# Kernel tuning notes

Measured on AMD Instinct MI355X. Metric: run time of the kernel, lower is better.

The kernel has to match this reference:

```python
import jax, jax.numpy as jnp
import numpy as np

POOL = 7; SR = 2; SCALE = 1.0 / 16
NUM_CLASSES = 21
NMS_THR = 0.5; MIN_SIZE = 1.0; TOPK = 100; SCORE_THR = 0.05
BBOX_CLIP = float(np.log(1000.0 / 16))


def roi_align(feat, rois):
    # feat: [C,H,W]; rois: [P,4] xyxy in image coords. torchvision aligned=True, sampling_ratio=2.
    C, H, W = feat.shape
    S = POOL * SR
    x0r = rois[:, 0] * SCALE - 0.5
    y0r = rois[:, 1] * SCALE - 0.5
    bw = (rois[:, 2] - rois[:, 0]) * SCALE / POOL
    bh = (rois[:, 3] - rois[:, 1]) * SCALE / POOL
    t = (jnp.arange(S, dtype=feat.dtype) + 0.5) / SR  # sample offsets in bin units
    ys = y0r[:, None] + bh[:, None] * t  # [P,S]
    xs = x0r[:, None] + bw[:, None] * t  # [P,S]
    vy = (ys >= -1.0) & (ys <= H)
    vx = (xs >= -1.0) & (xs <= W)
    y = jnp.clip(ys, 0.0, H - 1)
    x = jnp.clip(xs, 0.0, W - 1)
    yl = jnp.floor(y).astype(jnp.int32); xl = jnp.floor(x).astype(jnp.int32)
    yh = jnp.minimum(yl + 1, H - 1);     xh = jnp.minimum(xl + 1, W - 1)
    ly = y - yl; lx = x - xl
    hy = 1.0 - ly; hx = 1.0 - lx

    def g(Yi, Xi):  # -> [C,P,S,S]
        return feat[:, Yi[:, :, None], Xi[:, None, :]]

    val = (g(yl, xl) * (hy[:, :, None] * hx[:, None, :])
         + g(yl, xh) * (hy[:, :, None] * lx[:, None, :])
         + g(yh, xl) * (ly[:, :, None] * hx[:, None, :])
         + g(yh, xh) * (ly[:, :, None] * lx[:, None, :]))
    val = val * (vy[:, :, None] & vx[:, None, :])[None].astype(feat.dtype)
    P = rois.shape[0]
    val = val.reshape(C, P, POOL, SR, POOL, SR).mean(axis=(3, 5))  # avg over 2x2 samples/bin
    return val.transpose(1, 0, 2, 3)  # [P,C,POOL,POOL]


def decode(pred, proposals):
    # pred: [N,K,4] (dx,dy,dw,dh); proposals: [N,4]
    w = proposals[:, 2] - proposals[:, 0]
    h = proposals[:, 3] - proposals[:, 1]
    cx = proposals[:, 0] + 0.5 * w
    cy = proposals[:, 1] + 0.5 * h
    dx, dy = pred[..., 0], pred[..., 1]
    dw = jnp.minimum(pred[..., 2], BBOX_CLIP)
    dh = jnp.minimum(pred[..., 3], BBOX_CLIP)
    pcx = dx * w[:, None] + cx[:, None]
    pcy = dy * h[:, None] + cy[:, None]
    pw = jnp.exp(dw) * w[:, None]
    ph = jnp.exp(dh) * h[:, None]
    return jnp.stack([pcx - 0.5 * pw, pcy - 0.5 * ph, pcx + 0.5 * pw, pcy + 0.5 * ph], axis=-1)


def box_iou(b):
    x1, y1, x2, y2 = b[:, 0], b[:, 1], b[:, 2], b[:, 3]
    area = (x2 - x1) * (y2 - y1)
    iw = jnp.maximum(jnp.minimum(x2[:, None], x2[None, :]) - jnp.maximum(x1[:, None], x1[None, :]), 0.0)
    ih = jnp.maximum(jnp.minimum(y2[:, None], y2[None, :]) - jnp.maximum(y1[:, None], y1[None, :]), 0.0)
    inter = iw * ih
    return inter / (area[:, None] + area[None, :] - inter)


def filter_predictions(boxes, labels, scores):
    # score threshold + min-size + per-class greedy NMS + topK, static shapes (padded to TOPK)
    N = scores.shape[0]
    ws = boxes[:, 2] - boxes[:, 0]
    hs = boxes[:, 3] - boxes[:, 1]
    valid = (scores > SCORE_THR) & (ws >= MIN_SIZE) & (hs >= MIN_SIZE)
    skey = jnp.where(valid, scores, -jnp.inf)
    order = jnp.argsort(-skey)
    b = boxes[order]; s = skey[order]; l = labels[order]; v = valid[order]
    # batched_nms via per-class coordinate offset
    off = jax.lax.stop_gradient(jnp.max(boxes) + 1.0)
    ob = jax.lax.stop_gradient(b) + (l.astype(b.dtype) * off)[:, None]
    iou = box_iou(ob)  # [N,N]
    idx = jnp.arange(N)

    def body(keep, i):
        sup = (iou[i] > NMS_THR) & keep[i] & (idx > i)
        return keep & ~sup, None

    keep, _ = jax.lax.scan(body, v, idx)
    rank = jnp.cumsum(keep) - 1
    final = keep & (rank < TOPK)
    pick = jnp.argsort(jnp.where(final, idx, N))[:TOPK]  # kept indices in score order, padded
    ok = final[pick]
    out_boxes = jnp.where(ok[:, None], b[pick], 0.0)
    out_scores = jnp.where(ok, s[pick], 0.0)
    out_labels = jnp.where(ok, l[pick], -1)
    return out_boxes, out_labels, out_scores


def roi_head_forward(image, feat, proposals, fc6_w, fc6_b, fc7_w, fc7_b, cls_w, cls_b, reg_w, reg_b):
    H_img, W_img = image.shape[-2], image.shape[-1]
    pooled = roi_align(feat[0], proposals)  # [P,C,7,7]
    x = pooled.reshape(pooled.shape[0], -1)
    x = jax.nn.relu(x @ fc6_w.T + fc6_b)
    x = jax.nn.relu(x @ fc7_w.T + fc7_b)
    cls_scores = x @ cls_w.T + cls_b                       # [P,K]
    box_pred = (x @ reg_w.T + reg_b).reshape(-1, NUM_CLASSES, 4)
    boxes = decode(box_pred, proposals)                    # [P,K,4]
    scores = jax.nn.softmax(cls_scores, axis=-1)
    boxes = jnp.stack([boxes[..., 0].clip(0, W_img), boxes[..., 1].clip(0, H_img),
                       boxes[..., 2].clip(0, W_img), boxes[..., 3].clip(0, H_img)], axis=-1)
    labels = jnp.broadcast_to(jnp.arange(NUM_CLASSES), scores.shape)
    boxes = boxes[:, 1:].reshape(-1, 4)
    scores = scores[:, 1:].reshape(-1)
    labels = (labels[:, 1:] - 1).reshape(-1)
    return filter_predictions(boxes, labels, scores)


def setup_inputs() -> dict:
    key = jax.random.key(0)
    ks = jax.random.split(key, 12)
    H_img, W_img = 800, 1072
    P, C = 300, 512
    image = jnp.zeros((1, 3, H_img, W_img), jnp.float32)
    feat = jax.random.normal(ks[0], (1, C, H_img // 16, W_img // 16), jnp.float32)
    cx = jax.random.uniform(ks[1], (P,)) * W_img
    cy = jax.random.uniform(ks[2], (P,)) * H_img
    bw = 20.0 + jax.random.uniform(ks[3], (P,)) * 300.0
    bh = 20.0 + jax.random.uniform(ks[4], (P,)) * 300.0
    proposals = jnp.stack([jnp.clip(cx - bw / 2, 0, W_img), jnp.clip(cy - bh / 2, 0, H_img),
                           jnp.clip(cx + bw / 2, 0, W_img), jnp.clip(cy + bh / 2, 0, H_img)], axis=1)
    fin = C * POOL * POOL  # 25088
    D = 1024
    fc6_w = jax.random.normal(ks[5], (D, fin), jnp.float32) / np.sqrt(fin)
    fc6_b = jnp.zeros((D,), jnp.float32)
    fc7_w = jax.random.normal(ks[6], (D, D), jnp.float32) / np.sqrt(D)
    fc7_b = jnp.zeros((D,), jnp.float32)
    cls_w = jax.random.normal(ks[7], (NUM_CLASSES, D), jnp.float32) / np.sqrt(D)
    cls_b = jnp.zeros((NUM_CLASSES,), jnp.float32)
    reg_w = jax.random.normal(ks[8], (NUM_CLASSES * 4, D), jnp.float32) * 0.001
    reg_b = jnp.zeros((NUM_CLASSES * 4,), jnp.float32)
    return {"image": image, "feat": feat, "proposals": proposals,
            "fc6_w": fc6_w, "fc6_b": fc6_b, "fc7_w": fc7_w, "fc7_b": fc7_b,
            "cls_w": cls_w, "cls_b": cls_b, "reg_w": reg_w, "reg_b": reg_b}


def reference(image, feat, proposals, fc6_w, fc6_b, fc7_w, fc7_b, cls_w, cls_b, reg_w, reg_b):
    return roi_head_forward(image, feat, proposals, fc6_w, fc6_b, fc7_w, fc7_b, cls_w, cls_b, reg_w, reg_b)
```

## Files before the change

### kernel.cpp

```cpp
#include <hip/hip_runtime.h>
#include <hip/hip_bf16.h>
#include <math.h>

#define P_N   300
#define C_N   512
#define H_F   50
#define W_F   67
#define HW_F  3350
#define D_N   1024
#define FIN   25088
#define NCLS  21
#define NCAND 6000
#define W_IMG 1072.0f
#define H_IMG 800.0f
#define BBOX_CLIP_F 4.135166556742356f
#define KS6   42
#define STEPS6_PER_Z 19
#define KS7   16
#define STEPS7_PER_Z 2
#define KSH   16
#define STEPSH_PER_Z 2
#define NHEAD 128
#define NW    96
#define A_SCALE 16.0f
#define B_SCALE 256.0f
#define O_SCALE (1.0f / 4096.0f)

typedef __attribute__((ext_vector_type(8)))  _Float16 half8;
typedef __attribute__((ext_vector_type(16))) float    f32x16;

__device__ __forceinline__ void splitA(float f, _Float16& h, _Float16& l) {
  float fs = f * A_SCALE;
  h = (_Float16)fs;
  l = (_Float16)(fs - (float)h);
}

__global__ __launch_bounds__(256) void transpose_feat(const float* __restrict__ feat,
                                                      float* __restrict__ ft) {
  __shared__ float tile[32][33];
  const int s0 = blockIdx.x * 32, c0 = blockIdx.y * 32;
  const int tx = threadIdx.x, ty = threadIdx.y;
  for (int r = ty; r < 32; r += 8) {
    int c = c0 + r, s = s0 + tx;
    tile[r][tx] = (s < HW_F) ? feat[(size_t)c * HW_F + s] : 0.0f;
  }
  __syncthreads();
  for (int r = ty; r < 32; r += 8) {
    int s = s0 + r, c = c0 + tx;
    if (s < HW_F) ft[(size_t)s * C_N + c] = tile[tx][r];
  }
}

__global__ __launch_bounds__(256) void roi_align_k(const float* __restrict__ ft,
                                                   const float* __restrict__ rois,
                                                   _Float16* __restrict__ Xhi,
                                                   _Float16* __restrict__ Xlo) {
  __shared__ _Float16 hbuf[12544] __attribute__((aligned(16)));
  __shared__ _Float16 lbuf[12544] __attribute__((aligned(16)));
  __shared__ int   g_yl[14], g_yh[14], g_xl[14], g_xh[14];
  __shared__ float g_ly[14], g_hy[14], g_lx[14], g_hx[14];
  __shared__ int   g_vy[14], g_vx[14];

  const int p   = blockIdx.x;
  const int ch  = blockIdx.y;
  const int tid = threadIdx.x;

  if (tid < 14) {
    const float rx0 = rois[p*4+0], ry0 = rois[p*4+1], rx1 = rois[p*4+2], ry1 = rois[p*4+3];
    const float x0r = rx0 * 0.0625f - 0.5f;
    const float y0r = ry0 * 0.0625f - 0.5f;
    const float bw  = (rx1 - rx0) * 0.0625f * (1.0f / 7.0f);
    const float bh  = (ry1 - ry0) * 0.0625f * (1.0f / 7.0f);
    const float t   = ((float)tid + 0.5f) * 0.5f;

    const float ys = y0r + bh * t;
    g_vy[tid] = (ys >= -1.0f) && (ys <= (float)H_F);
    float y = fminf(fmaxf(ys, 0.0f), (float)(H_F - 1));
    int yi = (int)floorf(y);
    g_yl[tid] = yi; g_yh[tid] = min(yi + 1, H_F - 1);
    g_ly[tid] = y - (float)yi; g_hy[tid] = 1.0f - (y - (float)yi);

    const float xs = x0r + bw * t;
    g_vx[tid] = (xs >= -1.0f) && (xs <= (float)W_F);
    float x = fminf(fmaxf(xs, 0.0f), (float)(W_F - 1));
    int xi = (int)floorf(x);
    g_xl[tid] = xi; g_xh[tid] = min(xi + 1, W_F - 1);
    g_lx[tid] = x - (float)xi; g_hx[tid] = 1.0f - (x - (float)xi);
  }
  __syncthreads();

  const int c = ch * 256 + tid;
  for (int cell = 0; cell < 49; ++cell) {
    const int py = cell / 7;
    const int px = cell - py * 7;
    float acc = 0.0f;
#pragma unroll
    for (int sy = 0; sy < 2; ++sy) {
      const int iy = 2 * py + sy;
      if (!g_vy[iy]) continue;
      const float ly = g_ly[iy], hy = g_hy[iy];
      const int ry0i = g_yl[iy] * W_F, ry1i = g_yh[iy] * W_F;
#pragma unroll
      for (int sx = 0; sx < 2; ++sx) {
        const int ix = 2 * px + sx;
        if (!g_vx[ix]) continue;
        const float lx = g_lx[ix], hx = g_hx[ix];
        const float* b00 = ft + (size_t)(ry0i + g_xl[ix]) * C_N;
        const float* b01 = ft + (size_t)(ry0i + g_xh[ix]) * C_N;
        const float* b10 = ft + (size_t)(ry1i + g_xl[ix]) * C_N;
        const float* b11 = ft + (size_t)(ry1i + g_xh[ix]) * C_N;
        acc += (hy*hx)*b00[c] + (hy*lx)*b01[c] + (ly*hx)*b10[c] + (ly*lx)*b11[c];
      }
    }
    _Float16 h, l;
    splitA(acc * 0.25f, h, l);
    hbuf[tid * 49 + cell] = h;
    lbuf[tid * 49 + cell] = l;
  }
  __syncthreads();

  const size_t base = (size_t)p * FIN + (size_t)ch * 12544;
  const uint4* hs = (const uint4*)hbuf;
  const uint4* ls = (const uint4*)lbuf;
  uint4* dh = (uint4*)(Xhi + base);
  uint4* dl = (uint4*)(Xlo + base);
  for (int k = tid; k < 1568; k += 256) { dh[k] = hs[k]; dl[k] = ls[k]; }
}

__device__ __forceinline__ int swz(int slot, int ks) {
  return slot ^ ((slot >> 5) & 1) ^ (((slot >> 3) & 1) << 1) ^ ((ks & 1) << 2);
}

__global__ __launch_bounds__(256, 3) void gemm_f16_3p(
    const _Float16* __restrict__ Ahi, const _Float16* __restrict__ Alo,
    const float* __restrict__ Wt, float* __restrict__ Pt,
    int M, int K, int steps_per_z, int ldc)
{
  __shared__ _Float16 lds[16384];
  const int tid  = threadIdx.x;
  const int lane = tid & 63, wave = tid >> 6;
  const int wm = wave >> 1, wn = wave & 1;

  const int GX = gridDim.x, GY = gridDim.y;
  const int T  = GX * GY * gridDim.z;
  int flat = blockIdx.x + GX * (blockIdx.y + GY * blockIdx.z);
  if ((T & 7) == 0) flat = (flat & 7) * (T >> 3) + (flat >> 3);
  const int bx = flat % GX;
  const int by = (flat / GX) % GY;
  const int bz = flat / (GX * GY);

  const int m0 = bx * 128, n0 = by * 128;
  const int steps_total = K >> 5;
  const int s0 = bz * steps_per_z;
  const int s1 = min(s0 + steps_per_z, steps_total);

  f32x16 acc[2][2];
#pragma unroll
  for (int a = 0; a < 2; ++a)
#pragma unroll
    for (int b = 0; b < 2; ++b)
#pragma unroll
      for (int r = 0; r < 16; ++r) acc[a][b][r] = 0.f;

  const int srow = tid >> 2;
  const int j8   = tid & 3;
  const int ksW  = j8 >> 1, kc8 = j8 & 1;
  const int wslot = swz((kc8 << 5) | (srow & 31), ksW);

  for (int step = s0; step < s1; ++step) {
    const int kb = step << 5;
#pragma unroll
    for (int half = 0; half < 2; ++half) {
      const int row = srow + half * 64;
      const int mf  = row >> 5;
      const int gm  = m0 + row;
      uint4 vh = make_uint4(0,0,0,0), vl = make_uint4(0,0,0,0);
      if (gm < M) {
        vh = *reinterpret_cast<const uint4*>(Ahi + (size_t)gm * K + kb + j8 * 8);
        vl = *reinterpret_cast<const uint4*>(Alo + (size_t)gm * K + kb + j8 * 8);
      }
      const int base = (mf * 2 + ksW) * 512 + wslot * 8;
      *reinterpret_cast<uint4*>(&lds[base])        = vh;
      *reinterpret_cast<uint4*>(&lds[4096 + base]) = vl;
    }
#pragma unroll
    for (int half = 0; half < 2; ++half) {
      const int n = srow + half * 64;
      const float* wp = Wt + (size_t)(n0 + n) * K + kb + j8 * 8;
      const float4 f0 = *reinterpret_cast<const float4*>(wp);
      const float4 f1 = *reinterpret_cast<const float4*>(wp + 4);
      float fv[8] = {f0.x, f0.y, f0.z, f0.w, f1.x, f1.y, f1.z, f1.w};
      union { _Float16 h[8]; uint4 v; } uh, ul;
#pragma unroll
      for (int e = 0; e < 8; ++e) {
        float fs = fv[e] * B_SCALE;
        uh.h[e] = (_Float16)fs;
        ul.h[e] = (_Float16)(fs - (float)uh.h[e]);
      }
      const int nf = n >> 5;
      const int base = 8192 + (nf * 2 + ksW) * 512 + wslot * 8;
      *reinterpret_cast<uint4*>(&lds[base])        = uh.v;
      *reinterpret_cast<uint4*>(&lds[4096 + base]) = ul.v;
    }
    __syncthreads();
#pragma unroll
    for (int ks = 0; ks < 2; ++ks) {
      const int rslot = swz(lane, ks) * 8;
      half8 ah[2], al[2], bh[2], bl[2];
#pragma unroll
      for (int mi = 0; mi < 2; ++mi) {
        const int mf = wm * 2 + mi;
        ah[mi] = *reinterpret_cast<const half8*>(&lds[(mf * 2 + ks) * 512 + rslot]);
        al[mi] = *reinterpret_cast<const half8*>(&lds[4096 + (mf * 2 + ks) * 512 + rslot]);
      }
#pragma unroll
      for (int ni = 0; ni < 2; ++ni) {
        const int nf = wn * 2 + ni;
        bh[ni] = *reinterpret_cast<const half8*>(&lds[8192  + (nf * 2 + ks) * 512 + rslot]);
        bl[ni] = *reinterpret_cast<const half8*>(&lds[12288 + (nf * 2 + ks) * 512 + rslot]);
      }
#pragma unroll
      for (int mi = 0; mi < 2; ++mi)
#pragma unroll
        for (int ni = 0; ni < 2; ++ni) {
          acc[mi][ni] = __builtin_amdgcn_mfma_f32_32x32x16_f16(ah[mi], bh[ni], acc[mi][ni], 0, 0, 0);
          acc[mi][ni] = __builtin_amdgcn_mfma_f32_32x32x16_f16(ah[mi], bl[ni], acc[mi][ni], 0, 0, 0);
          acc[mi][ni] = __builtin_amdgcn_mfma_f32_32x32x16_f16(al[mi], bh[ni], acc[mi][ni], 0, 0, 0);
        }
    }
    __syncthreads();
  }
  const int col = lane & 31, rhi = lane >> 5;
  float* outp = Pt + (size_t)bz * ((size_t)M * ldc);
#pragma unroll
  for (int mi = 0; mi < 2; ++mi)
#pragma unroll
    for (int ni = 0; ni < 2; ++ni) {
      const int n = n0 + (wn * 2 + ni) * 32 + col;
      if (n >= ldc) continue;
#pragma unroll
      for (int r = 0; r < 16; ++r) {
        const int m = m0 + (wm * 2 + mi) * 32 + ((r & 3) + 8 * (r >> 2) + 4 * rhi);
        if (m < M) outp[(size_t)m * ldc + n] = acc[mi][ni][r] * O_SCALE;
      }
    }
}

__global__ __launch_bounds__(256) void reduce_bias(
    const float* __restrict__ Pt, const float* __restrict__ bias,
    float* __restrict__ out_f32, _Float16* __restrict__ out_hi, _Float16* __restrict__ out_lo,
    int MN, int KS, int nmask, int relu)
{
  int i = blockIdx.x * 256 + threadIdx.x;
  if (i >= MN) return;
  float s = 0.0f;
  for (int k = 0; k < KS; ++k) s += Pt[(size_t)k * MN + i];
  s += bias[i & nmask];
  if (relu) s = fmaxf(s, 0.0f);
  if (out_f32) out_f32[i] = s;
  if (out_hi) {
    _Float16 h, l; splitA(s, h, l);
    out_hi[i] = h; out_lo[i] = l;
  }
}

__global__ __launch_bounds__(256) void prep_head(const float* __restrict__ cls_w,
                                                 const float* __restrict__ cls_b,
                                                 const float* __restrict__ reg_w,
                                                 const float* __restrict__ reg_b,
                                                 float* __restrict__ Wpad,
                                                 float* __restrict__ bpad,
                                                 int* __restrict__ vcount) {
  const int row = blockIdx.x;
  const int t = threadIdx.x;
  if (row == 0 && t == 0) *vcount = 0;
  const float* src = (row < NCLS) ? (cls_w + (size_t)row * D_N)
                   : (row < 105)  ? (reg_w + (size_t)(row - NCLS) * D_N) : nullptr;
  float4 v = make_float4(0.f, 0.f, 0.f, 0.f);
  if (src) v = reinterpret_cast<const float4*>(src)[t];
  reinterpret_cast<float4*>(Wpad + (size_t)row * D_N)[t] = v;
  if (t == 0)
    bpad[row] = (row < NCLS) ? cls_b[row] : (row < 105) ? reg_b[row - NCLS] : 0.0f;
}

__global__ __launch_bounds__(64) void decode_kernel(const float* __restrict__ logits,
                                                    const float* __restrict__ props,
                                                    float* __restrict__ cboxes,
                                                    unsigned long long* __restrict__ ckeys,
                                                    int* __restrict__ vcount) {
  const int p = blockIdx.x;
  const int lane = threadIdx.x;
  const float* lg = logits + (size_t)p * NHEAD;

  float s = (lane < NCLS) ? lg[lane] : -__builtin_inff();
  float mx = s;
#pragma unroll
  for (int off = 32; off > 0; off >>= 1) mx = fmaxf(mx, __shfl_xor(mx, off));
  float e = (lane < NCLS) ? expf(s - mx) : 0.0f;
  float sum = e;
#pragma unroll
  for (int off = 32; off > 0; off >>= 1) sum += __shfl_xor(sum, off);
  const float sm = e / sum;

  if (lane >= 1 && lane < NCLS) {
    const int c = lane;
    const float x0 = props[p*4+0], y0 = props[p*4+1], x1 = props[p*4+2], y1 = props[p*4+3];
    const float w = x1 - x0, hh = y1 - y0;
    const float cx = x0 + 0.5f * w, cy = y0 + 0.5f * hh;
    const float dx = lg[NCLS + c*4 + 0];
    const float dy = lg[NCLS + c*4 + 1];
    const float dw = fminf(lg[NCLS + c*4 + 2], BBOX_CLIP_F);
    const float dh = fminf(lg[NCLS + c*4 + 3], BBOX_CLIP_F);
    const float pcx = dx * w + cx, pcy = dy * hh + cy;
    const float pw = expf(dw) * w, ph = expf(dh) * hh;
    float bx0 = pcx - 0.5f * pw, by0 = pcy - 0.5f * ph;
    float bx1 = pcx + 0.5f * pw, by1 = pcy + 0.5f * ph;
    bx0 = fminf(fmaxf(bx0, 0.0f), W_IMG);
    by0 = fminf(fmaxf(by0, 0.0f), H_IMG);
    bx1 = fminf(fmaxf(bx1, 0.0f), W_IMG);
    by1 = fminf(fmaxf(by1, 0.0f), H_IMG);
    const int idx = p * 20 + (c - 1);
    cboxes[idx*4+0] = bx0; cboxes[idx*4+1] = by0;
    cboxes[idx*4+2] = bx1; cboxes[idx*4+3] = by1;
    const bool valid = (sm > 0.05f) && ((bx1 - bx0) >= 1.0f) && ((by1 - by0) >= 1.0f);
    if (valid) {
      int pos = atomicAdd(vcount, 1);
      unsigned u = __float_as_uint(sm);
      ckeys[pos] = ((unsigned long long)(~u) << 32) | (unsigned)idx;
    }
  }
}

__global__ __launch_bounds__(1024) void sort_gather(const unsigned long long* __restrict__ ckeys,
                                                    const int* __restrict__ vcount,
                                                    const float* __restrict__ cboxes,
                                                    float4* __restrict__ sbox,
                                                    float* __restrict__ sscore,
                                                    int* __restrict__ slab) {
  __shared__ unsigned long long keys[8192];
  const int tid = threadIdx.x;
  const int V = *vcount;
  int Npad = 64; while (Npad < V) Npad <<= 1;
  for (int i = tid; i < Npad; i += 1024)
    keys[i] = (i < V) ? ckeys[i] : ~0ULL;
  __syncthreads();
  for (int kk = 2; kk <= Npad; kk <<= 1) {
    for (int j = kk >> 1; j > 0; j >>= 1) {
      for (int i = tid; i < Npad; i += 1024) {
        int ij = i ^ j;
        if (ij > i) {
          unsigned long long a = keys[i], b = keys[ij];
          bool up = ((i & kk) == 0);
          if ((a > b) == up) { keys[i] = b; keys[ij] = a; }
        }
      }
      __syncthreads();
    }
  }
  for (int i = tid; i < V; i += 1024) {
    unsigned long long key = keys[i];
    int idx = (int)(key & 0xffffffffu);
    sbox[i]   = *reinterpret_cast<const float4*>(&cboxes[(size_t)idx * 4]);
    sscore[i] = __uint_as_float(~(unsigned)(key >> 32));
    slab[i]   = idx % 20;
  }
}

__global__ __launch_bounds__(256) void iou_matrix(const float4* __restrict__ sbox,
                                                  const int* __restrict__ slab,
                                                  const int* __restrict__ vcount,
                                                  unsigned long long* __restrict__ mask) {
  const int V = *vcount;
  const int i = blockIdx.x * 4 + (threadIdx.x >> 6);
  const int lane = threadIdx.x & 63;
  if (i >= V) return;
  const float4 bi = sbox[i];
  const int li = slab[i];
  const float ai = (bi.z - bi.x) * (bi.w - bi.y);
  const int nw = (V + 63) >> 6;
  for (int w = 0; w < nw; ++w) {
    const int j = (w << 6) + lane;
    bool sup = false;
    if (j > i && j < V && slab[j] == li) {
      const float4 bj = sbox[j];
      const float iw = fminf(bi.z, bj.z) - fmaxf(bi.x, bj.x);
      const float ih = fminf(bi.w, bj.w) - fmaxf(bi.y, bj.y);
      const float inter = fmaxf(iw, 0.0f) * fmaxf(ih, 0.0f);
      const float aj = (bj.z - bj.x) * (bj.w - bj.y);
      sup = inter / (ai + aj - inter) > 0.5f;
    }
    const unsigned long long m = __ballot(sup);
    if (lane == 0) mask[(size_t)i * NW + w] = m;
  }
}

__device__ __forceinline__ unsigned long long bcast_live(unsigned long long live0,
                                                         unsigned long long live1, int w) {
  union { unsigned long long u; uint2 v; } t;
  t.u = (w < 64) ? live0 : live1;
  const int src = w & 63;
  const unsigned lo = __shfl(t.v.x, src);
  const unsigned hi = __shfl(t.v.y, src);
  return ((unsigned long long)hi << 32) | lo;
}

__global__ __launch_bounds__(64) void nms_scan(const float4* __restrict__ sbox,
                                               const float* __restrict__ sscore,
                                               const int* __restrict__ slab,
                                               const int* __restrict__ vcount,
                                               const unsigned long long* __restrict__ mask,
                                               float* __restrict__ out) {
  const int lane = threadIdx.x;
  const int V = min(*vcount, NCAND);
  const int nw = (V + 63) >> 6;
  unsigned long long live0 = ~0ULL, live1 = ~0ULL;
  int nk = 0;
  for (int w = 0; w < nw && nk < 100; ++w) {
    const int nb = V - (w << 6);
    const unsigned long long vmask = (nb >= 64) ? ~0ULL : ((1ULL << nb) - 1ULL);
    unsigned long long wv = bcast_live(live0, live1, w) & vmask;
    while (wv && nk < 100) {
      const int b = __ffsll((long long)wv) - 1;
      const int i = (w << 6) + b;
      if (lane == 0) {
        const float4 bb = sbox[i];
        out[nk*4+0] = bb.x; out[nk*4+1] = bb.y; out[nk*4+2] = bb.z; out[nk*4+3] = bb.w;
        out[400 + nk] = (float)slab[i];
        out[500 + nk] = sscore[i];
      }
      const unsigned long long* mrow = mask + (size_t)i * NW;
      if (lane < nw) live0 &= ~mrow[lane];
      if (64 + lane < nw) live1 &= ~mrow[64 + lane];
      nk++;
      wv = bcast_live(live0, live1, w) & vmask;
      wv &= (b == 63) ? 0ULL : ~((2ULL << b) - 1ULL);
    }
  }
  for (int r = nk + lane; r < 100; r += 64) {
    out[r*4+0] = 0.0f; out[r*4+1] = 0.0f; out[r*4+2] = 0.0f; out[r*4+3] = 0.0f;
    out[400 + r] = -1.0f;
    out[500 + r] = 0.0f;
  }
}

extern "C" void kernel_launch(void* const* d_in, const int* in_sizes, int n_in,
                              void* d_out, int out_size, void* d_ws, size_t ws_size,
                              hipStream_t stream) {
  const float* feat   = (const float*)d_in[1];
  const float* props  = (const float*)d_in[2];
  const float* fc6_w  = (const float*)d_in[3];
  const float* fc6_b  = (const float*)d_in[4];
  const float* fc7_w  = (const float*)d_in[5];
  const float* fc7_b  = (const float*)d_in[6];
  const float* cls_w  = (const float*)d_in[7];
  const float* cls_b  = (const float*)d_in[8];
  const float* reg_w  = (const float*)d_in[9];
  const float* reg_b  = (const float*)d_in[10];

  char* ws = (char*)d_ws;
  size_t off = 0;
  auto alloc = [&](size_t bytes) -> void* {
    void* p = ws + off;
    off += (bytes + 255) & ~(size_t)255;
    return p;
  };

  _Float16* Xhi  = (_Float16*)alloc((size_t)P_N * FIN * 2);
  _Float16* Xlo  = (_Float16*)alloc((size_t)P_N * FIN * 2);
  float*    Pt   = (float*)alloc((size_t)KS6 * P_N * D_N * 4);
  _Float16* h6hi = (_Float16*)alloc((size_t)P_N * D_N * 2);
  _Float16* h6lo = (_Float16*)alloc((size_t)P_N * D_N * 2);
  _Float16* h7hi = (_Float16*)alloc((size_t)P_N * D_N * 2);
  _Float16* h7lo = (_Float16*)alloc((size_t)P_N * D_N * 2);
  float*    Wpad = (float*)alloc((size_t)NHEAD * D_N * 4);
  float*    bpad = (float*)alloc((size_t)NHEAD * 4);
  float*  logits = (float*)alloc((size_t)P_N * NHEAD * 4);
  float*  cboxes = (float*)alloc((size_t)NCAND * 4 * 4);
  unsigned long long* ckeys = (unsigned long long*)alloc((size_t)NCAND * 8);
  float4*   sbox = (float4*)alloc((size_t)NCAND * 16);
  float*  sscore = (float*)alloc((size_t)NCAND * 4);
  int*      slab = (int*)alloc((size_t)NCAND * 4);
  unsigned long long* supmask = (unsigned long long*)alloc((size_t)NCAND * NW * 8);
  int*    vcount = (int*)alloc(256);
  float* ft = Pt;
  (void)ws_size; (void)in_sizes; (void)n_in; (void)out_size;

  prep_head<<<NHEAD, 256, 0, stream>>>(cls_w, cls_b, reg_w, reg_b, Wpad, bpad, vcount);
  transpose_feat<<<dim3((HW_F + 31) / 32, C_N / 32), dim3(32, 8), 0, stream>>>(feat, ft);
  roi_align_k<<<dim3(P_N, 2), 256, 0, stream>>>(ft, props, Xhi, Xlo);
  gemm_f16_3p<<<dim3(3, 8, KS6), 256, 0, stream>>>(Xhi, Xlo, fc6_w, Pt, P_N, FIN, STEPS6_PER_Z, D_N);
  reduce_bias<<<(P_N * D_N + 255) / 256, 256, 0, stream>>>(
      Pt, fc6_b, nullptr, h6hi, h6lo, P_N * D_N, KS6, D_N - 1, 1);
  gemm_f16_3p<<<dim3(3, 8, KS7), 256, 0, stream>>>(h6hi, h6lo, fc7_w, Pt, P_N, D_N, STEPS7_PER_Z, D_N);
  reduce_bias<<<(P_N * D_N + 255) / 256, 256, 0, stream>>>(
      Pt, fc7_b, nullptr, h7hi, h7lo, P_N * D_N, KS7, D_N - 1, 1);
  gemm_f16_3p<<<dim3(3, 1, KSH), 256, 0, stream>>>(h7hi, h7lo, Wpad, Pt, P_N, D_N, STEPSH_PER_Z, NHEAD);
  reduce_bias<<<(P_N * NHEAD + 255) / 256, 256, 0, stream>>>(
      Pt, bpad, logits, nullptr, nullptr, P_N * NHEAD, KSH, NHEAD - 1, 0);
  decode_kernel<<<P_N, 64, 0, stream>>>(logits, props, cboxes, ckeys, vcount);
  sort_gather<<<1, 1024, 0, stream>>>(ckeys, vcount, cboxes, sbox, sscore, slab);
  iou_matrix<<<(NCAND + 3) / 4, 256, 0, stream>>>(sbox, slab, vcount, supmask);
  nms_scan<<<1, 64, 0, stream>>>(sbox, sscore, slab, vcount, supmask, (float*)d_out);
}
```

Before: 343.2 us.

## Fuse tail into single-block kernel, prefetch GEMM stages, halve fc6 split-K

Merges the head-weight padding into the feature transpose launch. Fuses decode, sort, IoU matrix and NMS scan into one 1024-thread kernel that runs greedy NMS from registers with block barriers and drops the suppression-mask matrix. Adds register double-buffering of global loads in the split-K GEMM. Halves the fc6 split-K factor to shrink partial-sum traffic. In exchange, NMS is now serialized with two block syncs per kept box, and the fc6 GEMM launches fewer blocks.

New measurement: 761.6 us. +121.9%, slower.

```diff
diff --git a/kernel.cpp b/kernel.cpp
--- a/kernel.cpp
+++ b/kernel.cpp
@@ -14,17 +14,17 @@
 #define W_IMG 1072.0f
 #define H_IMG 800.0f
 #define BBOX_CLIP_F 4.135166556742356f
-#define KS6   42
-#define STEPS6_PER_Z 19
+#define KS6   21
+#define STEPS6_PER_Z 38
 #define KS7   16
 #define STEPS7_PER_Z 2
 #define KSH   16
 #define STEPSH_PER_Z 2
 #define NHEAD 128
-#define NW    96
 #define A_SCALE 16.0f
 #define B_SCALE 256.0f
 #define O_SCALE (1.0f / 4096.0f)
+#define TBLK  1680
 
 typedef __attribute__((ext_vector_type(8)))  _Float16 half8;
 typedef __attribute__((ext_vector_type(16))) float    f32x16;
@@ -35,19 +35,39 @@
   l = (_Float16)(fs - (float)h);
 }
 
-__global__ __launch_bounds__(256) void transpose_feat(const float* __restrict__ feat,
-                                                      float* __restrict__ ft) {
+__global__ __launch_bounds__(256) void prep_transpose(const float* __restrict__ feat,
+                                                      float* __restrict__ ft,
+                                                      const float* __restrict__ cls_w,
+                                                      const float* __restrict__ cls_b,
+                                                      const float* __restrict__ reg_w,
+                                                      const float* __restrict__ reg_b,
+                                                      float* __restrict__ Wpad,
+                                                      float* __restrict__ bpad) {
   __shared__ float tile[32][33];
-  const int s0 = blockIdx.x * 32, c0 = blockIdx.y * 32;
-  const int tx = threadIdx.x, ty = threadIdx.y;
-  for (int r = ty; r < 32; r += 8) {
-    int c = c0 + r, s = s0 + tx;
-    tile[r][tx] = (s < HW_F) ? feat[(size_t)c * HW_F + s] : 0.0f;
-  }
-  __syncthreads();
-  for (int r = ty; r < 32; r += 8) {
-    int s = s0 + r, c = c0 + tx;
-    if (s < HW_F) ft[(size_t)s * C_N + c] = tile[tx][r];
+  const int bid = blockIdx.x;
+  const int tid = threadIdx.x;
+  if (bid < TBLK) {
+    const int bx = bid % 105, byy = bid / 105;
+    const int s0 = bx * 32, c0 = byy * 32;
+    const int tx = tid & 31, ty = tid >> 5;
+    for (int r = ty; r < 32; r += 8) {
+      int c = c0 + r, s = s0 + tx;
+      tile[r][tx] = (s < HW_F) ? feat[(size_t)c * HW_F + s] : 0.0f;
+    }
+    __syncthreads();
+    for (int r = ty; r < 32; r += 8) {
+      int s = s0 + r, c = c0 + tx;
+      if (s < HW_F) ft[(size_t)s * C_N + c] = tile[tx][r];
+    }
+  } else {
+    const int row = bid - TBLK;
+    const float* src = (row < NCLS) ? (cls_w + (size_t)row * D_N)
+                     : (row < 105)  ? (reg_w + (size_t)(row - NCLS) * D_N) : nullptr;
+    float4 v = make_float4(0.f, 0.f, 0.f, 0.f);
+    if (src) v = reinterpret_cast<const float4*>(src)[tid];
+    reinterpret_cast<float4*>(Wpad + (size_t)row * D_N)[tid] = v;
+    if (tid == 0)
+      bpad[row] = (row < NCLS) ? cls_b[row] : (row < 105) ? reg_b[row - NCLS] : 0.0f;
   }
 }
 
@@ -131,6 +151,58 @@
   return slot ^ ((slot >> 5) & 1) ^ (((slot >> 3) & 1) << 1) ^ ((ks & 1) << 2);
 }
 
+struct SReg { uint4 ah0, ah1, al0, al1; float4 b00, b01, b10, b11; };
+
+__device__ __forceinline__ void stage_load(SReg& R, const _Float16* __restrict__ Ahi,
+                                           const _Float16* __restrict__ Alo,
+                                           const float* __restrict__ Wt,
+                                           int M, int K, int m0, int n0,
+                                           int srow, int j8, int kb) {
+  const int gm0 = m0 + srow, gm1 = m0 + srow + 64;
+  R.ah0 = make_uint4(0,0,0,0); R.al0 = R.ah0; R.ah1 = R.ah0; R.al1 = R.ah0;
+  if (gm0 < M) {
+    R.ah0 = *reinterpret_cast<const uint4*>(Ahi + (size_t)gm0 * K + kb + j8 * 8);
+    R.al0 = *reinterpret_cast<const uint4*>(Alo + (size_t)gm0 * K + kb + j8 * 8);
+  }
+  if (gm1 < M) {
+    R.ah1 = *reinterpret_cast<const uint4*>(Ahi + (size_t)gm1 * K + kb + j8 * 8);
+    R.al1 = *reinterpret_cast<const uint4*>(Alo + (size_t)gm1 * K + kb + j8 * 8);
+  }
+  const float* wp0 = Wt + (size_t)(n0 + srow) * K + kb + j8 * 8;
+  const float* wp1 = Wt + (size_t)(n0 + srow + 64) * K + kb + j8 * 8;
+  R.b00 = *reinterpret_cast<const float4*>(wp0);
+  R.b01 = *reinterpret_cast<const float4*>(wp0 + 4);
+  R.b10 = *reinterpret_cast<const float4*>(wp1);
+  R.b11 = *reinterpret_cast<const float4*>(wp1 + 4);
+}
+
+__device__ __forceinline__ void stage_write(const SReg& R, _Float16* lds,
+                                            int srow, int ksW, int wslot) {
+  const int mf0 = srow >> 5, mf1 = (srow + 64) >> 5;
+  const int base0 = (mf0 * 2 + ksW) * 512 + wslot * 8;
+  const int base1 = (mf1 * 2 + ksW) * 512 + wslot * 8;
+  *reinterpret_cast<uint4*>(&lds[base0])        = R.ah0;
+  *reinterpret_cast<uint4*>(&lds[4096 + base0]) = R.al0;
+  *reinterpret_cast<uint4*>(&lds[base1])        = R.ah1;
+  *reinterpret_cast<uint4*>(&lds[4096 + base1]) = R.al1;
+  float fv0[8] = {R.b00.x, R.b00.y, R.b00.z, R.b00.w, R.b01.x, R.b01.y, R.b01.z, R.b01.w};
+  float fv1[8] = {R.b10.x, R.b10.y, R.b10.z, R.b10.w, R.b11.x, R.b11.y, R.b11.z, R.b11.w};
+  union { _Float16 h[8]; uint4 v; } uh0, ul0, uh1, ul1;
+#pragma unroll
+  for (int e = 0; e < 8; ++e) {
+    float fs0 = fv0[e] * B_SCALE;
+    uh0.h[e] = (_Float16)fs0;
+    ul0.h[e] = (_Float16)(fs0 - (float)uh0.h[e]);
+    float fs1 = fv1[e] * B_SCALE;
+    uh1.h[e] = (_Float16)fs1;
+    ul1.h[e] = (_Float16)(fs1 - (float)uh1.h[e]);
+  }
+  *reinterpret_cast<uint4*>(&lds[8192  + base0]) = uh0.v;
+  *reinterpret_cast<uint4*>(&lds[12288 + base0]) = ul0.v;
+  *reinterpret_cast<uint4*>(&lds[8192  + base1]) = uh1.v;
+  *reinterpret_cast<uint4*>(&lds[12288 + base1]) = ul1.v;
+}
+
 __global__ __launch_bounds__(256, 3) void gemm_f16_3p(
     const _Float16* __restrict__ Ahi, const _Float16* __restrict__ Alo,
     const float* __restrict__ Wt, float* __restrict__ Pt,
@@ -167,42 +239,7 @@
   const int ksW  = j8 >> 1, kc8 = j8 & 1;
   const int wslot = swz((kc8 << 5) | (srow & 31), ksW);
 
-  for (int step = s0; step < s1; ++step) {
-    const int kb = step << 5;
-#pragma unroll
-    for (int half = 0; half < 2; ++half) {
-      const int row = srow + half * 64;
-      const int mf  = row >> 5;
-      const int gm  = m0 + row;
-      uint4 vh = make_uint4(0,0,0,0), vl = make_uint4(0,0,0,0);
-      if (gm < M) {
-        vh = *reinterpret_cast<const uint4*>(Ahi + (size_t)gm * K + kb + j8 * 8);
-        vl = *reinterpret_cast<const uint4*>(Alo + (size_t)gm * K + kb + j8 * 8);
-      }
-      const int base = (mf * 2 + ksW) * 512 + wslot * 8;
-      *reinterpret_cast<uint4*>(&lds[base])        = vh;
-      *reinterpret_cast<uint4*>(&lds[4096 + base]) = vl;
-    }
-#pragma unroll
-    for (int half = 0; half < 2; ++half) {
-      const int n = srow + half * 64;
-      const float* wp = Wt + (size_t)(n0 + n) * K + kb + j8 * 8;
-      const float4 f0 = *reinterpret_cast<const float4*>(wp);
-      const float4 f1 = *reinterpret_cast<const float4*>(wp + 4);
-      float fv[8] = {f0.x, f0.y, f0.z, f0.w, f1.x, f1.y, f1.z, f1.w};
-      union { _Float16 h[8]; uint4 v; } uh, ul;
-#pragma unroll
-      for (int e = 0; e < 8; ++e) {
-        float fs = fv[e] * B_SCALE;
-        uh.h[e] = (_Float16)fs;
-        ul.h[e] = (_Float16)(fs - (float)uh.h[e]);
-      }
-      const int nf = n >> 5;
-      const int base = 8192 + (nf * 2 + ksW) * 512 + wslot * 8;
-      *reinterpret_cast<uint4*>(&lds[base])        = uh.v;
-      *reinterpret_cast<uint4*>(&lds[4096 + base]) = ul.v;
-    }
-    __syncthreads();
+  auto compute = [&]() {
 #pragma unroll
     for (int ks = 0; ks < 2; ++ks) {
       const int rslot = swz(lane, ks) * 8;
@@ -228,8 +265,25 @@
           acc[mi][ni] = __builtin_amdgcn_mfma_f32_32x32x16_f16(al[mi], bh[ni], acc[mi][ni], 0, 0, 0);
         }
     }
+  };
+
+  SReg R0, R1;
+  if (s0 < s1) stage_load(R0, Ahi, Alo, Wt, M, K, m0, n0, srow, j8, s0 << 5);
+  for (int s = s0; s < s1; s += 2) {
+    if (s + 1 < s1) stage_load(R1, Ahi, Alo, Wt, M, K, m0, n0, srow, j8, (s + 1) << 5);
+    stage_write(R0, lds, srow, ksW, wslot);
     __syncthreads();
-  }
+    compute();
+    __syncthreads();
+    if (s + 1 < s1) {
+      if (s + 2 < s1) stage_load(R0, Ahi, Alo, Wt, M, K, m0, n0, srow, j8, (s + 2) << 5);
+      stage_write(R1, lds, srow, ksW, wslot);
+      __syncthreads();
+      compute();
+      __syncthreads();
+    }
+  }
+
   const int col = lane & 31, rhi = lane >> 5;
   float* outp = Pt + (size_t)bz * ((size_t)M * ldc);
 #pragma unroll
@@ -264,47 +318,47 @@
   }
 }
 
-__global__ __launch_bounds__(256) void prep_head(const float* __restrict__ cls_w,
-                                                 const float* __restrict__ cls_b,
-                                                 const float* __restrict__ reg_w,
-                                                 const float* __restrict__ reg_b,
-                                                 float* __restrict__ Wpad,
-                                                 float* __restrict__ bpad,
-                                                 int* __restrict__ vcount) {
-  const int row = blockIdx.x;
-  const int t = threadIdx.x;
-  if (row == 0 && t == 0) *vcount = 0;
-  const float* src = (row < NCLS) ? (cls_w + (size_t)row * D_N)
-                   : (row < 105)  ? (reg_w + (size_t)(row - NCLS) * D_N) : nullptr;
-  float4 v = make_float4(0.f, 0.f, 0.f, 0.f);
-  if (src) v = reinterpret_cast<const float4*>(src)[t];
-  reinterpret_cast<float4*>(Wpad + (size_t)row * D_N)[t] = v;
-  if (t == 0)
-    bpad[row] = (row < NCLS) ? cls_b[row] : (row < 105) ? reg_b[row - NCLS] : 0.0f;
-}
-
-__global__ __launch_bounds__(64) void decode_kernel(const float* __restrict__ logits,
+__global__ __launch_bounds__(1024) void tail_kernel(const float* __restrict__ logits,
                                                     const float* __restrict__ props,
                                                     float* __restrict__ cboxes,
-                                                    unsigned long long* __restrict__ ckeys,
-                                                    int* __restrict__ vcount) {
-  const int p = blockIdx.x;
-  const int lane = threadIdx.x;
-  const float* lg = logits + (size_t)p * NHEAD;
-
-  float s = (lane < NCLS) ? lg[lane] : -__builtin_inff();
-  float mx = s;
-#pragma unroll
-  for (int off = 32; off > 0; off >>= 1) mx = fmaxf(mx, __shfl_xor(mx, off));
-  float e = (lane < NCLS) ? expf(s - mx) : 0.0f;
-  float sum = e;
-#pragma unroll
-  for (int off = 32; off > 0; off >>= 1) sum += __shfl_xor(sum, off);
-  const float sm = e / sum;
-
-  if (lane >= 1 && lane < NCLS) {
-    const int c = lane;
-    const float x0 = props[p*4+0], y0 = props[p*4+1], x1 = props[p*4+2], y1 = props[p*4+3];
+                                                    float* __restrict__ out) {
+  __shared__ unsigned long long keys[8192];
+  __shared__ float sc_lds[NCAND];
+  __shared__ float pr_lds[P_N * 4];
+  __shared__ int sh_v;
+  __shared__ int sh_next;
+  __shared__ float4 sh_pbox;
+  __shared__ int sh_plab;
+  const int tid = threadIdx.x;
+
+  if (tid == 0) sh_v = 0;
+  for (int i = tid; i < P_N * 4; i += 1024) pr_lds[i] = props[i];
+  __syncthreads();
+
+  if (tid < P_N) {
+    const float* lg = logits + (size_t)tid * NHEAD;
+    float mx = lg[0];
+#pragma unroll
+    for (int c = 1; c < NCLS; ++c) mx = fmaxf(mx, lg[c]);
+    float sum = 0.0f;
+#pragma unroll
+    for (int c = 0; c < NCLS; ++c) {
+      float e = expf(lg[c] - mx);
+      sum += e;
+      if (c >= 1) sc_lds[tid * 20 + (c - 1)] = e;
+    }
+    float inv = 1.0f / sum;
+#pragma unroll
+    for (int c = 1; c < NCLS; ++c) sc_lds[tid * 20 + (c - 1)] *= inv;
+  }
+  __syncthreads();
+
+  for (int i = tid; i < NCAND; i += 1024) {
+    const int p = i / 20;
+    const int l = i - p * 20;
+    const int c = l + 1;
+    const float* lg = logits + (size_t)p * NHEAD;
+    const float x0 = pr_lds[p*4+0], y0 = pr_lds[p*4+1], x1 = pr_lds[p*4+2], y1 = pr_lds[p*4+3];
     const float w = x1 - x0, hh = y1 - y0;
     const float cx = x0 + 0.5f * w, cy = y0 + 0.5f * hh;
     const float dx = lg[NCLS + c*4 + 0];
@@ -319,31 +373,21 @@
     by0 = fminf(fmaxf(by0, 0.0f), H_IMG);
     bx1 = fminf(fmaxf(bx1, 0.0f), W_IMG);
     by1 = fminf(fmaxf(by1, 0.0f), H_IMG);
-    const int idx = p * 20 + (c - 1);
-    cboxes[idx*4+0] = bx0; cboxes[idx*4+1] = by0;
-    cboxes[idx*4+2] = bx1; cboxes[idx*4+3] = by1;
+    *reinterpret_cast<float4*>(cboxes + (size_t)i * 4) = make_float4(bx0, by0, bx1, by1);
+    const float sm = sc_lds[i];
     const bool valid = (sm > 0.05f) && ((bx1 - bx0) >= 1.0f) && ((by1 - by0) >= 1.0f);
     if (valid) {
-      int pos = atomicAdd(vcount, 1);
+      int pos = atomicAdd(&sh_v, 1);
       unsigned u = __float_as_uint(sm);
-      ckeys[pos] = ((unsigned long long)(~u) << 32) | (unsigned)idx;
-    }
-  }
-}
-
-__global__ __launch_bounds__(1024) void sort_gather(const unsigned long long* __restrict__ ckeys,
-                                                    const int* __restrict__ vcount,
-                                                    const float* __restrict__ cboxes,
-                                                    float4* __restrict__ sbox,
-                                                    float* __restrict__ sscore,
-                                                    int* __restrict__ slab) {
-  __shared__ unsigned long long keys[8192];
-  const int tid = threadIdx.x;
-  const int V = *vcount;
+      keys[pos] = ((unsigned long long)(~u) << 32) | (unsigned)i;
+    }
+  }
+  __syncthreads();
+  const int V = sh_v;
   int Npad = 64; while (Npad < V) Npad <<= 1;
-  for (int i = tid; i < Npad; i += 1024)
-    keys[i] = (i < V) ? ckeys[i] : ~0ULL;
+  for (int i = V + tid; i < Npad; i += 1024) keys[i] = ~0ULL;
   __syncthreads();
+
   for (int kk = 2; kk <= Npad; kk <<= 1) {
     for (int j = kk >> 1; j > 0; j >>= 1) {
       for (int i = tid; i < Npad; i += 1024) {
@@ -357,86 +401,63 @@
       __syncthreads();
     }
   }
-  for (int i = tid; i < V; i += 1024) {
-    unsigned long long key = keys[i];
-    int idx = (int)(key & 0xffffffffu);
-    sbox[i]   = *reinterpret_cast<const float4*>(&cboxes[(size_t)idx * 4]);
-    sscore[i] = __uint_as_float(~(unsigned)(key >> 32));
-    slab[i]   = idx % 20;
-  }
-}
-
-__global__ __launch_bounds__(256) void iou_matrix(const float4* __restrict__ sbox,
-                                                  const int* __restrict__ slab,
-                                                  const int* __restrict__ vcount,
-                                                  unsigned long long* __restrict__ mask) {
-  const int V = *vcount;
-  const int i = blockIdx.x * 4 + (threadIdx.x >> 6);
-  const int lane = threadIdx.x & 63;
-  if (i >= V) return;
-  const float4 bi = sbox[i];
-  const int li = slab[i];
-  const float ai = (bi.z - bi.x) * (bi.w - bi.y);
-  const int nw = (V + 63) >> 6;
-  for (int w = 0; w < nw; ++w) {
-    const int j = (w << 6) + lane;
-    bool sup = false;
-    if (j > i && j < V && slab[j] == li) {
-      const float4 bj = sbox[j];
-      const float iw = fminf(bi.z, bj.z) - fmaxf(bi.x, bj.x);
-      const float ih = fminf(bi.w, bj.w) - fmaxf(bi.y, bj.y);
-      const float inter = fmaxf(iw, 0.0f) * fmaxf(ih, 0.0f);
-      const float aj = (bj.z - bj.x) * (bj.w - bj.y);
-      sup = inter / (ai + aj - inter) > 0.5f;
-    }
-    const unsigned long long m = __ballot(sup);
-    if (lane == 0) mask[(size_t)i * NW + w] = m;
-  }
-}
-
-__device__ __forceinline__ unsigned long long bcast_live(unsigned long long live0,
-                                                         unsigned long long live1, int w) {
-  union { unsigned long long u; uint2 v; } t;
-  t.u = (w < 64) ? live0 : live1;
-  const int src = w & 63;
-  const unsigned lo = __shfl(t.v.x, src);
-  const unsigned hi = __shfl(t.v.y, src);
-  return ((unsigned long long)hi << 32) | lo;
-}
-
-__global__ __launch_bounds__(64) void nms_scan(const float4* __restrict__ sbox,
-                                               const float* __restrict__ sscore,
-                                               const int* __restrict__ slab,
-                                               const int* __restrict__ vcount,
-                                               const unsigned long long* __restrict__ mask,
-                                               float* __restrict__ out) {
-  const int lane = threadIdx.x;
-  const int V = min(*vcount, NCAND);
-  const int nw = (V + 63) >> 6;
-  unsigned long long live0 = ~0ULL, live1 = ~0ULL;
+
+  float4 bx[6]; float sscr[6]; int lb[6], gi[6]; bool lv[6];
+#pragma unroll
+  for (int s = 0; s < 6; ++s) {
+    const int g = s * 1024 + tid;
+    lv[s] = false; gi[s] = 0x7fffffff; lb[s] = -1;
+    bx[s] = make_float4(0.f, 0.f, 0.f, 0.f); sscr[s] = 0.f;
+    if (g < V) {
+      const unsigned long long key = keys[g];
+      const int idx = (int)(key & 0xffffffffu);
+      bx[s] = *reinterpret_cast<const float4*>(cboxes + (size_t)idx * 4);
+      sscr[s] = __uint_as_float(~(unsigned)(key >> 32));
+      lb[s] = idx % 20;
+      gi[s] = g; lv[s] = true;
+    }
+  }
+
   int nk = 0;
-  for (int w = 0; w < nw && nk < 100; ++w) {
-    const int nb = V - (w << 6);
-    const unsigned long long vmask = (nb >= 64) ? ~0ULL : ((1ULL << nb) - 1ULL);
-    unsigned long long wv = bcast_live(live0, live1, w) & vmask;
-    while (wv && nk < 100) {
-      const int b = __ffsll((long long)wv) - 1;
-      const int i = (w << 6) + b;
-      if (lane == 0) {
-        const float4 bb = sbox[i];
-        out[nk*4+0] = bb.x; out[nk*4+1] = bb.y; out[nk*4+2] = bb.z; out[nk*4+3] = bb.w;
-        out[400 + nk] = (float)slab[i];
-        out[500 + nk] = sscore[i];
-      }
-      const unsigned long long* mrow = mask + (size_t)i * NW;
-      if (lane < nw) live0 &= ~mrow[lane];
-      if (64 + lane < nw) live1 &= ~mrow[64 + lane];
-      nk++;
-      wv = bcast_live(live0, live1, w) & vmask;
-      wv &= (b == 63) ? 0ULL : ~((2ULL << b) - 1ULL);
-    }
-  }
-  for (int r = nk + lane; r < 100; r += 64) {
+  int cur = 0;
+  while (cur < V && nk < 100) {
+    if (tid == 0) sh_next = 0x7fffffff;
+#pragma unroll
+    for (int s = 0; s < 6; ++s) {
+      if (lv[s] && gi[s] == cur) {
+        sh_pbox = bx[s]; sh_plab = lb[s];
+        out[nk*4+0] = bx[s].x; out[nk*4+1] = bx[s].y;
+        out[nk*4+2] = bx[s].z; out[nk*4+3] = bx[s].w;
+        out[400 + nk] = (float)lb[s];
+        out[500 + nk] = sscr[s];
+        lv[s] = false;
+      }
+    }
+    __syncthreads();
+    const float4 pb = sh_pbox;
+    const int pl = sh_plab;
+    const float pa = (pb.z - pb.x) * (pb.w - pb.y);
+    int mn = 0x7fffffff;
+#pragma unroll
+    for (int s = 0; s < 6; ++s) {
+      if (lv[s]) {
+        if (lb[s] == pl) {
+          const float iw = fminf(pb.z, bx[s].z) - fmaxf(pb.x, bx[s].x);
+          const float ih = fminf(pb.w, bx[s].w) - fmaxf(pb.y, bx[s].y);
+          const float inter = fmaxf(iw, 0.0f) * fmaxf(ih, 0.0f);
+          const float aj = (bx[s].z - bx[s].x) * (bx[s].w - bx[s].y);
+          if (inter / (pa + aj - inter) > 0.5f) lv[s] = false;
+        }
+        if (lv[s]) mn = min(mn, gi[s]);
+      }
+    }
+    if (mn != 0x7fffffff) atomicMin(&sh_next, mn);
+    __syncthreads();
+    cur = sh_next;
+    nk++;
+  }
+
+  for (int r = nk + tid; r < 100; r += 1024) {
     out[r*4+0] = 0.0f; out[r*4+1] = 0.0f; out[r*4+2] = 0.0f; out[r*4+3] = 0.0f;
     out[400 + r] = -1.0f;
     out[500 + r] = 0.0f;
@@ -476,17 +497,11 @@
   float*    bpad = (float*)alloc((size_t)NHEAD * 4);
   float*  logits = (float*)alloc((size_t)P_N * NHEAD * 4);
   float*  cboxes = (float*)alloc((size_t)NCAND * 4 * 4);
-  unsigned long long* ckeys = (unsigned long long*)alloc((size_t)NCAND * 8);
-  float4*   sbox = (float4*)alloc((size_t)NCAND * 16);
-  float*  sscore = (float*)alloc((size_t)NCAND * 4);
-  int*      slab = (int*)alloc((size_t)NCAND * 4);
-  unsigned long long* supmask = (unsigned long long*)alloc((size_t)NCAND * NW * 8);
-  int*    vcount = (int*)alloc(256);
   float* ft = Pt;
   (void)ws_size; (void)in_sizes; (void)n_in; (void)out_size;
 
-  prep_head<<<NHEAD, 256, 0, stream>>>(cls_w, cls_b, reg_w, reg_b, Wpad, bpad, vcount);
-  transpose_feat<<<dim3((HW_F + 31) / 32, C_N / 32), dim3(32, 8), 0, stream>>>(feat, ft);
+  prep_transpose<<<TBLK + NHEAD, 256, 0, stream>>>(feat, ft, cls_w, cls_b, reg_w, reg_b,
+                                                   Wpad, bpad);
   roi_align_k<<<dim3(P_N, 2), 256, 0, stream>>>(ft, props, Xhi, Xlo);
   gemm_f16_3p<<<dim3(3, 8, KS6), 256, 0, stream>>>(Xhi, Xlo, fc6_w, Pt, P_N, FIN, STEPS6_PER_Z, D_N);
   reduce_bias<<<(P_N * D_N + 255) / 256, 256, 0, stream>>>(
@@ -497,8 +512,5 @@
   gemm_f16_3p<<<dim3(3, 1, KSH), 256, 0, stream>>>(h7hi, h7lo, Wpad, Pt, P_N, D_N, STEPSH_PER_Z, NHEAD);
   reduce_bias<<<(P_N * NHEAD + 255) / 256, 256, 0, stream>>>(
       Pt, bpad, logits, nullptr, nullptr, P_N * NHEAD, KSH, NHEAD - 1, 0);
-  decode_kernel<<<P_N, 64, 0, stream>>>(logits, props, cboxes, ckeys, vcount);
-  sort_gather<<<1, 1024, 0, stream>>>(ckeys, vcount, cboxes, sbox, sscore, slab);
-  iou_matrix<<<(NCAND + 3) / 4, 256, 0, stream>>>(sbox, slab, vcount, supmask);
-  nms_scan<<<1, 64, 0, stream>>>(sbox, sscore, slab, vcount, supmask, (float*)d_out);
-}
+  tail_kernel<<<1, 1024, 0, stream>>>(logits, props, cboxes, (float*)d_out);
+}
```
